# Optimization experiments

Measured on AMD Instinct MI355X. Metric: run time of the kernel, lower is better.

## Reference

```python
import jax, jax.numpy as jnp
import numpy as np

EPS = 1e-10            # safe_log epsilon
SIGMOID_BETA = 1.0
MLE_STEP_SIZE = 0.01
NUM_MLE_STEPS = 15
ENT_MULT = 0.01        # entropy loss multiplier placeholder
DECAY_MULT = 0.001     # weight decay multiplier placeholder
B, P, N, T = 512, 1024, 1024, 32


def sigmoid(a, beta=SIGMOID_BETA):
    # module's rescaled sigmoid: 2/(1+exp(-beta*a)) - 1, range (-1, 1)
    return 2.0 / (1.0 + jnp.exp(-beta * a)) - 1.0


def tri_basis(a_sig, centers):
    # triangle basis functions: relu(1 - |a - c_j| / width), width = center spacing
    # a_sig [B,N], centers [T] -> [B,N,T]
    width = centers[1] - centers[0]
    return jax.nn.relu(1.0 - jnp.abs(a_sig[..., None] - centers) / width)


def prob_est(a_sig, thetas, centers):
    # per-neuron mixture of triangle kernels; mixture weights = softmax(thetas)
    pi = jax.nn.softmax(thetas, axis=1)               # [N,T]
    return jnp.einsum('bnt,nt->bn', tri_basis(a_sig, centers), pi)  # [B,N]


def log_likelihood(a_sig, thetas, centers):
    return jnp.sum(jnp.log(prob_est(a_sig, thetas, centers) + EPS))


def calc_entropy(probs):
    # per-neuron entropy reduction over the batch axis
    return -jnp.sum(probs * jnp.log(probs + EPS), axis=0)  # [N]


def setup_inputs() -> dict:
    key = jax.random.key(0)
    k0, k1, k2, k3 = jax.random.split(key, 4)
    x = jax.random.normal(k0, (B, P), jnp.float32)
    w_enc = 0.5 * jax.random.normal(k1, (P, N), jnp.float32)   # truncated_normal std 0.5 approx
    b_enc = 0.1 * jax.random.normal(k2, (N,), jnp.float32)
    w_dec = jnp.transpose(w_enc)                                # initialized as w_enc^T
    b_dec = 0.1 * jax.random.normal(k3, (P,), jnp.float32)
    thetas = jnp.ones((N, T), jnp.float32)                      # construct_thetas init
    triangle_centers = jnp.linspace(-1.0, 1.0, T).astype(jnp.float32)  # a_sig range
    return {"x": x, "w_enc": w_enc, "b_enc": b_enc, "w_dec": w_dec,
            "b_dec": b_dec, "thetas": thetas, "triangle_centers": triangle_centers}


def reference(x, w_enc, b_enc, w_dec, b_dec, thetas, triangle_centers):
    # --- inference: relu encoder (noise_var_mult = 0 -> deterministic a) ---
    a = jax.nn.relu(x @ w_enc + b_enc)                # [B,N]
    a_sig = sigmoid(a, SIGMOID_BETA)                  # [B,N] in (-1,1)

    # --- iterative MLE gradient-ascent on thetas (num_mle_steps updates) ---
    ll_grad = jax.grad(lambda th: log_likelihood(a_sig, th, triangle_centers))

    def mle_step(th, _):
        return th + MLE_STEP_SIZE * ll_grad(th), None

    thetas_new, _ = jax.lax.scan(mle_step, thetas, None, length=NUM_MLE_STEPS)

    # --- entropy of the triangle-kernel density estimate ---
    probs = prob_est(a_sig, thetas_new, triangle_centers)   # [B,N]
    a_entropies = calc_entropy(probs)                       # [N]

    # --- decoder / losses ---
    x_hat = a @ w_dec + b_dec                               # [B,P]
    recon_loss = jnp.mean(0.5 * jnp.sum((x - x_hat) ** 2, axis=1))
    entropy_loss = ENT_MULT * jnp.sum(a_entropies)
    # tf.nn.l2_loss(t) = sum(t^2)/2
    decay_loss = 0.5 * DECAY_MULT * (0.5 * jnp.sum(w_enc ** 2) + 0.5 * jnp.sum(w_dec ** 2))
    total_loss = recon_loss + entropy_loss + decay_loss
    return x_hat, a_entropies, total_loss
```

## Files before the change

### kernel.cpp

```cpp
#include <hip/hip_runtime.h>

#define EPSC 1e-10f
#define BDIM 512
#define PDIM 1024
#define NDIM 1024
#define TDIM 32

typedef __attribute__((ext_vector_type(8))) short short8;
typedef __attribute__((ext_vector_type(4))) float f32x4;

static __device__ __forceinline__ short f2bf(float f) {
  unsigned u = __float_as_uint(f);
  unsigned r = (u + 0x7fffu + ((u >> 16) & 1u)) >> 16;
  return (short)r;
}

__global__ __launch_bounds__(256) void conv_x_kernel(
    const float* __restrict__ X, short* __restrict__ Xbf, float* __restrict__ accums)
{
  int tid = threadIdx.x;
  if (blockIdx.x == 0 && tid < 4) accums[tid] = 0.0f;
  size_t base = (size_t)blockIdx.x * 2048 + (size_t)tid * 8;
  float4 v0 = *(const float4*)(X + base);
  float4 v1 = *(const float4*)(X + base + 4);
  short8 o;
  o[0] = f2bf(v0.x); o[1] = f2bf(v0.y); o[2] = f2bf(v0.z); o[3] = f2bf(v0.w);
  o[4] = f2bf(v1.x); o[5] = f2bf(v1.y); o[6] = f2bf(v1.z); o[7] = f2bf(v1.w);
  *(short8*)(Xbf + base) = o;
}

__global__ __launch_bounds__(256) void conv_w_kernel(
    const float* __restrict__ W1, const float* __restrict__ W2,
    short* __restrict__ T1, short* __restrict__ T2, float* __restrict__ accums)
{
  __shared__ float T[64][65];
  __shared__ float red[4];
  const float* src = blockIdx.z ? W2 : W1;
  short* dst = blockIdx.z ? T2 : T1;
  int tid = threadIdx.x;
  int r0 = blockIdx.y * 64;
  int c0 = blockIdx.x * 64;
  float wsq = 0.0f;
#pragma unroll
  for (int i = 0; i < 4; ++i) {
    int row = (tid >> 4) + i * 16;
    int col = (tid & 15) << 2;
    float4 v = *(const float4*)(src + (size_t)(r0 + row) * NDIM + c0 + col);
    T[row][col + 0] = v.x; T[row][col + 1] = v.y; T[row][col + 2] = v.z; T[row][col + 3] = v.w;
    wsq = fmaf(v.x, v.x, wsq); wsq = fmaf(v.y, v.y, wsq);
    wsq = fmaf(v.z, v.z, wsq); wsq = fmaf(v.w, v.w, wsq);
  }
  __syncthreads();
  int n = tid >> 2;
  int kb = (tid & 3) << 4;
  short8 o0, o1;
#pragma unroll
  for (int i = 0; i < 8; ++i) o0[i] = f2bf(T[kb + i][n]);
#pragma unroll
  for (int i = 0; i < 8; ++i) o1[i] = f2bf(T[kb + 8 + i][n]);
  short* dp = dst + (size_t)(c0 + n) * NDIM + r0 + kb;
  *(short8*)dp = o0;
  *(short8*)(dp + 8) = o1;
#pragma unroll
  for (int d = 32; d >= 1; d >>= 1) wsq += __shfl_xor(wsq, d);
  if ((tid & 63) == 0) red[tid >> 6] = wsq;
  __syncthreads();
  if (tid == 0) atomicAdd(accums + 2, red[0] + red[1] + red[2] + red[3]);
}

__global__ __launch_bounds__(256) void gemm1_mfma(
    const short* __restrict__ Xbf, const short* __restrict__ WT,
    const float* __restrict__ bias, const float* __restrict__ centers,
    short* __restrict__ Abf, float* __restrict__ U)
{
  int tid = threadIdx.x;
  int lane = tid & 63, wid = tid >> 6;
  int q = lane >> 4, r16 = lane & 15;
  int bn = blockIdx.x * 32;
  int m = blockIdx.y * 64 + wid * 16 + r16;
  const short* ap  = Xbf + (size_t)m * NDIM + q * 8;
  const short* b0p = WT + (size_t)(bn + r16) * NDIM + q * 8;
  const short* b1p = b0p + 16 * NDIM;
  f32x4 acc0 = {0.f, 0.f, 0.f, 0.f};
  f32x4 acc1 = {0.f, 0.f, 0.f, 0.f};
#pragma unroll 4
  for (int k = 0; k < NDIM; k += 32) {
    short8 a  = *(const short8*)(ap + k);
    short8 b0 = *(const short8*)(b0p + k);
    short8 b1 = *(const short8*)(b1p + k);
    acc0 = __builtin_amdgcn_mfma_f32_16x16x32_bf16(a, b0, acc0, 0, 0, 0);
    acc1 = __builtin_amdgcn_mfma_f32_16x16x32_bf16(a, b1, acc1, 0, 0, 0);
  }
  float c0 = centers[0];
  float invw = 1.0f / (centers[1] - centers[0]);
  int mrow = blockIdx.y * 64 + wid * 16 + (q << 2);
  int n0 = bn + r16;
  float bi0 = bias[n0], bi1 = bias[n0 + 16];
#pragma unroll
  for (int r = 0; r < 4; ++r) {
    int mm = mrow + r;
    float a0 = fmaxf(acc0[r] + bi0, 0.0f);
    float a1 = fmaxf(acc1[r] + bi1, 0.0f);
    Abf[(size_t)mm * NDIM + n0]      = f2bf(a0);
    Abf[(size_t)mm * NDIM + n0 + 16] = f2bf(a1);
    U[(size_t)n0 * BDIM + mm]        = (2.0f / (1.0f + __expf(-a0)) - 1.0f - c0) * invw;
    U[(size_t)(n0 + 16) * BDIM + mm] = (2.0f / (1.0f + __expf(-a1)) - 1.0f - c0) * invw;
  }
}

__global__ __launch_bounds__(256) void gemm2_mfma(
    const short* __restrict__ Abf, const short* __restrict__ WdT,
    const float* __restrict__ bias, const float* __restrict__ X,
    float* __restrict__ out, float* __restrict__ accums)
{
  __shared__ float red[4];
  int tid = threadIdx.x;
  int lane = tid & 63, wid = tid >> 6;
  int q = lane >> 4, r16 = lane & 15;
  int bn = blockIdx.x * 32;
  int m = blockIdx.y * 64 + wid * 16 + r16;
  const short* ap  = Abf + (size_t)m * NDIM + q * 8;
  const short* b0p = WdT + (size_t)(bn + r16) * NDIM + q * 8;
  const short* b1p = b0p + 16 * NDIM;
  f32x4 acc0 = {0.f, 0.f, 0.f, 0.f};
  f32x4 acc1 = {0.f, 0.f, 0.f, 0.f};
#pragma unroll 4
  for (int k = 0; k < NDIM; k += 32) {
    short8 a  = *(const short8*)(ap + k);
    short8 b0 = *(const short8*)(b0p + k);
    short8 b1 = *(const short8*)(b1p + k);
    acc0 = __builtin_amdgcn_mfma_f32_16x16x32_bf16(a, b0, acc0, 0, 0, 0);
    acc1 = __builtin_amdgcn_mfma_f32_16x16x32_bf16(a, b1, acc1, 0, 0, 0);
  }
  int mrow = blockIdx.y * 64 + wid * 16 + (q << 2);
  int p0 = bn + r16;
  float bi0 = bias[p0], bi1 = bias[p0 + 16];
  float local = 0.0f;
#pragma unroll
  for (int r = 0; r < 4; ++r) {
    int mm = mrow + r;
    float xh0 = acc0[r] + bi0;
    float xh1 = acc1[r] + bi1;
    out[(size_t)mm * PDIM + p0]      = xh0;
    out[(size_t)mm * PDIM + p0 + 16] = xh1;
    float d0 = xh0 - X[(size_t)mm * PDIM + p0];
    float d1 = xh1 - X[(size_t)mm * PDIM + p0 + 16];
    local = fmaf(d0, d0, local);
    local = fmaf(d1, d1, local);
  }
#pragma unroll
  for (int d = 32; d >= 1; d >>= 1) local += __shfl_xor(local, d);
  if ((tid & 63) == 0) red[tid >> 6] = local;
  __syncthreads();
  if (tid == 0) atomicAdd(accums + 0, red[0] + red[1] + red[2] + red[3]);
}

__global__ __launch_bounds__(64) void mle_kernel(
    const float* __restrict__ U, const float* __restrict__ thetas,
    float* __restrict__ ent_out, float* __restrict__ accums)
{
  int n = blockIdx.x;
  int lane = threadIdx.x;
  __shared__ float th_s[TDIM];
  __shared__ float pi_s[TDIM];
  __shared__ float s_s[64 * 33];

  float f_reg[8];
  int j_reg[8];
#pragma unroll
  for (int i = 0; i < 8; i++) {
    float u = U[(size_t)n * BDIM + lane + i * 64];
    int j = (int)u;
    if (j > TDIM - 2) j = TDIM - 2;
    f_reg[i] = u - (float)j;
    j_reg[i] = j;
  }
  if (lane < TDIM) th_s[lane] = thetas[(size_t)n * TDIM + lane];
  __syncthreads();

  int h = lane >> 5, t = lane & 31;
  for (int step = 0; step < 15; ++step) {
    float tv = th_s[lane & 31];
    float mx = tv;
#pragma unroll
    for (int d = 16; d >= 1; d >>= 1) mx = fmaxf(mx, __shfl_xor(mx, d));
    float e = __expf(tv - mx);
    float se = e;
#pragma unroll
    for (int d = 16; d >= 1; d >>= 1) se += __shfl_xor(se, d);
    float pv = e / se;
    if (lane < TDIM) pi_s[lane] = pv;
#pragma unroll
    for (int i = 0; i < 33; i++) s_s[lane * 33 + i] = 0.0f;
    __syncthreads();

    float S_local = 0.0f;
#pragma unroll
    for (int i = 0; i < 8; i++) {
      int j = j_reg[i];
      float f = f_reg[i];
      float p = (1.0f - f) * pi_s[j] + f * pi_s[j + 1];
      float r = 1.0f / (p + EPSC);
      S_local = fmaf(p, r, S_local);
      float* sp = &s_s[lane * 33 + j];
      sp[0] += (1.0f - f) * r;
      sp[1] += f * r;
    }
    __syncthreads();
    float S = S_local;
#pragma unroll
    for (int d = 32; d >= 1; d >>= 1) S += __shfl_xor(S, d);
    float colsum = 0.0f;
#pragma unroll 8
    for (int L = 0; L < 32; ++L) colsum += s_s[(h * 32 + L) * 33 + t];
    colsum += __shfl_xor(colsum, 32);
    if (lane < TDIM) th_s[lane] += 0.01f * pv * (colsum - S);
    __syncthreads();
  }

  float tv = th_s[lane & 31];
  float mx = tv;
#pragma unroll
  for (int d = 16; d >= 1; d >>= 1) mx = fmaxf(mx, __shfl_xor(mx, d));
  float e = __expf(tv - mx);
  float se = e;
#pragma unroll
  for (int d = 16; d >= 1; d >>= 1) se += __shfl_xor(se, d);
  if (lane < TDIM) pi_s[lane] = e / se;
  __syncthreads();
  float ent_local = 0.0f;
#pragma unroll
  for (int i = 0; i < 8; i++) {
    int j = j_reg[i];
    float f = f_reg[i];
    float p = (1.0f - f) * pi_s[j] + f * pi_s[j + 1];
    ent_local = fmaf(p, __logf(p + EPSC), ent_local);
  }
  float E = ent_local;
#pragma unroll
  for (int d = 32; d >= 1; d >>= 1) E += __shfl_xor(E, d);
  if (lane == 0) {
    float entn = -E;
    ent_out[n] = entn;
    atomicAdd(accums + 1, entn);
  }
}

__global__ void finalize_kernel(const float* __restrict__ accums, float* __restrict__ out) {
  if (threadIdx.x == 0) {
    float recon = accums[0] * (0.5f / (float)BDIM);
    float entl = 0.01f * accums[1];
    float decay = 0.00025f * accums[2];
    out[(size_t)BDIM * PDIM + NDIM] = recon + entl + decay;
  }
}

extern "C" void kernel_launch(void* const* d_in, const int* in_sizes, int n_in,
                              void* d_out, int out_size, void* d_ws, size_t ws_size,
                              hipStream_t stream) {
  (void)in_sizes; (void)n_in; (void)out_size; (void)ws_size;
  const float* x       = (const float*)d_in[0];
  const float* w_enc   = (const float*)d_in[1];
  const float* b_enc   = (const float*)d_in[2];
  const float* w_dec   = (const float*)d_in[3];
  const float* b_dec   = (const float*)d_in[4];
  const float* thetas  = (const float*)d_in[5];
  const float* centers = (const float*)d_in[6];
  float* out = (float*)d_out;

  char* ws = (char*)d_ws;
  short* Xbf    = (short*)(ws);
  short* WT     = (short*)(ws + (1 << 20));
  short* WdT    = (short*)(ws + (3 << 20));
  short* Abf    = (short*)(ws + (5 << 20));
  float* accums = (float*)(ws + (6 << 20));
  float* U      = out;
  float* ent_out = out + (size_t)BDIM * PDIM;

  hipLaunchKernelGGL(conv_x_kernel, dim3(256), dim3(256), 0, stream, x, Xbf, accums);
  hipLaunchKernelGGL(conv_w_kernel, dim3(16, 16, 2), dim3(256), 0, stream,
                     w_enc, w_dec, WT, WdT, accums);
  hipLaunchKernelGGL(gemm1_mfma, dim3(32, 8), dim3(256), 0, stream,
                     Xbf, WT, b_enc, centers, Abf, U);
  hipLaunchKernelGGL(mle_kernel, dim3(NDIM), dim3(64), 0, stream, U, thetas, ent_out, accums);
  hipLaunchKernelGGL(gemm2_mfma, dim3(32, 8), dim3(256), 0, stream,
                     Abf, WdT, b_dec, x, out, accums);
  hipLaunchKernelGGL(finalize_kernel, dim3(1), dim3(64), 0, stream, accums, out);
}
```

Baseline: 152.4 us.

## Swizzle operands into MFMA fragment layout, merge conversions, and finalize loss via ticket

Converts X and both weight matrices in a single launch into a pre-swizzled tile layout that matches MFMA fragment order, so each GEMM lane reads one contiguous short8 per k-chunk. The GEMMs are retiled to one 16x16 tile per wave, doubling the grid. U now goes to workspace and is written through a shared-memory transpose with float4 stores. The MLE kernel drops shared-memory pi/theta buffers in favour of shuffles and uses a wider padded scratch layout. Atomics and the separate finalize kernel are replaced by per-block partial sums plus a last-block ticket reduction, removing two launches. The cost is more complex indexing and a ticket counter that gemm1 resets on every call.

New measurement: 159.0 us. +4.3%, slower.

```diff
diff --git a/kernel.cpp b/kernel.cpp
--- a/kernel.cpp
+++ b/kernel.cpp
@@ -15,31 +15,33 @@
   return (short)r;
 }
 
-__global__ __launch_bounds__(256) void conv_x_kernel(
-    const float* __restrict__ X, short* __restrict__ Xbf, float* __restrict__ accums)
+__global__ __launch_bounds__(256) void conv_kernel(
+    const float* __restrict__ X, const float* __restrict__ W1, const float* __restrict__ W2,
+    short* __restrict__ Xsw, short* __restrict__ T1, short* __restrict__ T2,
+    float* __restrict__ pwsq)
 {
   int tid = threadIdx.x;
-  if (blockIdx.x == 0 && tid < 4) accums[tid] = 0.0f;
-  size_t base = (size_t)blockIdx.x * 2048 + (size_t)tid * 8;
-  float4 v0 = *(const float4*)(X + base);
-  float4 v1 = *(const float4*)(X + base + 4);
-  short8 o;
-  o[0] = f2bf(v0.x); o[1] = f2bf(v0.y); o[2] = f2bf(v0.z); o[3] = f2bf(v0.w);
-  o[4] = f2bf(v1.x); o[5] = f2bf(v1.y); o[6] = f2bf(v1.z); o[7] = f2bf(v1.w);
-  *(short8*)(Xbf + base) = o;
-}
-
-__global__ __launch_bounds__(256) void conv_w_kernel(
-    const float* __restrict__ W1, const float* __restrict__ W2,
-    short* __restrict__ T1, short* __restrict__ T2, float* __restrict__ accums)
-{
+  if (blockIdx.x < 256) {
+    int i = blockIdx.x * 256 + tid;
+    int m = i >> 7, c = i & 127;
+    const float* src = X + (size_t)m * 1024 + c * 8;
+    float4 v0 = *(const float4*)src;
+    float4 v1 = *(const float4*)(src + 4);
+    short8 o;
+    o[0] = f2bf(v0.x); o[1] = f2bf(v0.y); o[2] = f2bf(v0.z); o[3] = f2bf(v0.w);
+    o[4] = f2bf(v1.x); o[5] = f2bf(v1.y); o[6] = f2bf(v1.z); o[7] = f2bf(v1.w);
+    *(short8*)(Xsw + ((size_t)((m >> 4) * 32 + (c >> 2)) * 512) + (c & 3) * 128 + (m & 15) * 8) = o;
+    return;
+  }
   __shared__ float T[64][65];
   __shared__ float red[4];
-  const float* src = blockIdx.z ? W2 : W1;
-  short* dst = blockIdx.z ? T2 : T1;
-  int tid = threadIdx.x;
-  int r0 = blockIdx.y * 64;
-  int c0 = blockIdx.x * 64;
+  int wb = blockIdx.x - 256;
+  int z = wb >> 8;
+  int w = wb & 255;
+  int r0 = (w >> 4) * 64;
+  int c0 = (w & 15) * 64;
+  const float* src = z ? W2 : W1;
+  short* dst = z ? T2 : T1;
   float wsq = 0.0f;
 #pragma unroll
   for (int i = 0; i < 4; ++i) {
@@ -51,119 +53,115 @@
     wsq = fmaf(v.z, v.z, wsq); wsq = fmaf(v.w, v.w, wsq);
   }
   __syncthreads();
-  int n = tid >> 2;
+  int nl = tid >> 2;
   int kb = (tid & 3) << 4;
-  short8 o0, o1;
-#pragma unroll
-  for (int i = 0; i < 8; ++i) o0[i] = f2bf(T[kb + i][n]);
-#pragma unroll
-  for (int i = 0; i < 8; ++i) o1[i] = f2bf(T[kb + 8 + i][n]);
-  short* dp = dst + (size_t)(c0 + n) * NDIM + r0 + kb;
-  *(short8*)dp = o0;
-  *(short8*)(dp + 8) = o1;
+  int ng = c0 + nl;
+  int nt = ng >> 4, rn = ng & 15;
+#pragma unroll
+  for (int h = 0; h < 2; ++h) {
+    int kg = r0 + kb + 8 * h;
+    int kc = kg >> 5, q = (kg >> 3) & 3;
+    short8 o;
+#pragma unroll
+    for (int e = 0; e < 8; ++e) o[e] = f2bf(T[kb + 8 * h + e][nl]);
+    *(short8*)(dst + ((size_t)(nt * 32 + kc) * 512) + q * 128 + rn * 8) = o;
+  }
 #pragma unroll
   for (int d = 32; d >= 1; d >>= 1) wsq += __shfl_xor(wsq, d);
   if ((tid & 63) == 0) red[tid >> 6] = wsq;
   __syncthreads();
-  if (tid == 0) atomicAdd(accums + 2, red[0] + red[1] + red[2] + red[3]);
+  if (tid == 0) pwsq[wb] = red[0] + red[1] + red[2] + red[3];
 }
 
 __global__ __launch_bounds__(256) void gemm1_mfma(
-    const short* __restrict__ Xbf, const short* __restrict__ WT,
+    const short* __restrict__ Xsw, const short* __restrict__ Wsw,
     const float* __restrict__ bias, const float* __restrict__ centers,
-    short* __restrict__ Abf, float* __restrict__ U)
-{
+    short* __restrict__ Absw, float* __restrict__ U, int* __restrict__ ticket)
+{
+  __shared__ float T2s[32][36];
   int tid = threadIdx.x;
+  if (blockIdx.x == 0 && blockIdx.y == 0 && tid == 0) *ticket = 0;
   int lane = tid & 63, wid = tid >> 6;
-  int q = lane >> 4, r16 = lane & 15;
-  int bn = blockIdx.x * 32;
-  int m = blockIdx.y * 64 + wid * 16 + r16;
-  const short* ap  = Xbf + (size_t)m * NDIM + q * 8;
-  const short* b0p = WT + (size_t)(bn + r16) * NDIM + q * 8;
-  const short* b1p = b0p + 16 * NDIM;
-  f32x4 acc0 = {0.f, 0.f, 0.f, 0.f};
-  f32x4 acc1 = {0.f, 0.f, 0.f, 0.f};
-#pragma unroll 4
-  for (int k = 0; k < NDIM; k += 32) {
-    short8 a  = *(const short8*)(ap + k);
-    short8 b0 = *(const short8*)(b0p + k);
-    short8 b1 = *(const short8*)(b1p + k);
-    acc0 = __builtin_amdgcn_mfma_f32_16x16x32_bf16(a, b0, acc0, 0, 0, 0);
-    acc1 = __builtin_amdgcn_mfma_f32_16x16x32_bf16(a, b1, acc1, 0, 0, 0);
-  }
+  int wy = wid >> 1, wx = wid & 1;
+  int mt = blockIdx.y * 2 + wy;
+  int nt = blockIdx.x * 2 + wx;
+  const short* ap = Xsw + (size_t)mt * 16384 + lane * 8;
+  const short* bp = Wsw + (size_t)nt * 16384 + lane * 8;
+  f32x4 acc = {0.f, 0.f, 0.f, 0.f};
+#pragma unroll 8
+  for (int kc = 0; kc < 32; ++kc) {
+    short8 a = *(const short8*)(ap + kc * 512);
+    short8 b = *(const short8*)(bp + kc * 512);
+    acc = __builtin_amdgcn_mfma_f32_16x16x32_bf16(a, b, acc, 0, 0, 0);
+  }
+  int q = lane >> 4, r = lane & 15;
+  int nn = nt * 16 + r;
+  float bi = bias[nn];
   float c0 = centers[0];
   float invw = 1.0f / (centers[1] - centers[0]);
-  int mrow = blockIdx.y * 64 + wid * 16 + (q << 2);
-  int n0 = bn + r16;
-  float bi0 = bias[n0], bi1 = bias[n0 + 16];
-#pragma unroll
-  for (int r = 0; r < 4; ++r) {
-    int mm = mrow + r;
-    float a0 = fmaxf(acc0[r] + bi0, 0.0f);
-    float a1 = fmaxf(acc1[r] + bi1, 0.0f);
-    Abf[(size_t)mm * NDIM + n0]      = f2bf(a0);
-    Abf[(size_t)mm * NDIM + n0 + 16] = f2bf(a1);
-    U[(size_t)n0 * BDIM + mm]        = (2.0f / (1.0f + __expf(-a0)) - 1.0f - c0) * invw;
-    U[(size_t)(n0 + 16) * BDIM + mm] = (2.0f / (1.0f + __expf(-a1)) - 1.0f - c0) * invw;
-  }
+  short* abase = Absw + ((size_t)(mt * 32 + (nn >> 5)) * 512) + ((nn >> 3) & 3) * 128 + (nn & 7);
+#pragma unroll
+  for (int rr = 0; rr < 4; ++rr) {
+    int rm = q * 4 + rr;
+    float a = fmaxf(acc[rr] + bi, 0.0f);
+    abase[rm * 8] = f2bf(a);
+    T2s[wx * 16 + r][wy * 16 + rm] = (2.0f / (1.0f + __expf(-a)) - 1.0f - c0) * invw;
+  }
+  __syncthreads();
+  int row = tid >> 3;
+  int col4 = (tid & 7) << 2;
+  float4 uv = make_float4(T2s[row][col4], T2s[row][col4 + 1], T2s[row][col4 + 2], T2s[row][col4 + 3]);
+  *(float4*)(U + (size_t)(blockIdx.x * 32 + row) * BDIM + blockIdx.y * 32 + col4) = uv;
 }
 
 __global__ __launch_bounds__(256) void gemm2_mfma(
-    const short* __restrict__ Abf, const short* __restrict__ WdT,
+    const short* __restrict__ Absw, const short* __restrict__ Wdsw,
     const float* __restrict__ bias, const float* __restrict__ X,
-    float* __restrict__ out, float* __restrict__ accums)
+    float* __restrict__ out, float* __restrict__ precon)
 {
   __shared__ float red[4];
   int tid = threadIdx.x;
   int lane = tid & 63, wid = tid >> 6;
-  int q = lane >> 4, r16 = lane & 15;
-  int bn = blockIdx.x * 32;
-  int m = blockIdx.y * 64 + wid * 16 + r16;
-  const short* ap  = Abf + (size_t)m * NDIM + q * 8;
-  const short* b0p = WdT + (size_t)(bn + r16) * NDIM + q * 8;
-  const short* b1p = b0p + 16 * NDIM;
-  f32x4 acc0 = {0.f, 0.f, 0.f, 0.f};
-  f32x4 acc1 = {0.f, 0.f, 0.f, 0.f};
-#pragma unroll 4
-  for (int k = 0; k < NDIM; k += 32) {
-    short8 a  = *(const short8*)(ap + k);
-    short8 b0 = *(const short8*)(b0p + k);
-    short8 b1 = *(const short8*)(b1p + k);
-    acc0 = __builtin_amdgcn_mfma_f32_16x16x32_bf16(a, b0, acc0, 0, 0, 0);
-    acc1 = __builtin_amdgcn_mfma_f32_16x16x32_bf16(a, b1, acc1, 0, 0, 0);
-  }
-  int mrow = blockIdx.y * 64 + wid * 16 + (q << 2);
-  int p0 = bn + r16;
-  float bi0 = bias[p0], bi1 = bias[p0 + 16];
+  int wy = wid >> 1, wx = wid & 1;
+  int mt = blockIdx.y * 2 + wy;
+  int nt = blockIdx.x * 2 + wx;
+  const short* ap = Absw + (size_t)mt * 16384 + lane * 8;
+  const short* bp = Wdsw + (size_t)nt * 16384 + lane * 8;
+  f32x4 acc = {0.f, 0.f, 0.f, 0.f};
+#pragma unroll 8
+  for (int kc = 0; kc < 32; ++kc) {
+    short8 a = *(const short8*)(ap + kc * 512);
+    short8 b = *(const short8*)(bp + kc * 512);
+    acc = __builtin_amdgcn_mfma_f32_16x16x32_bf16(a, b, acc, 0, 0, 0);
+  }
+  int q = lane >> 4, r = lane & 15;
+  int nn = nt * 16 + r;
+  float bi = bias[nn];
   float local = 0.0f;
 #pragma unroll
-  for (int r = 0; r < 4; ++r) {
-    int mm = mrow + r;
-    float xh0 = acc0[r] + bi0;
-    float xh1 = acc1[r] + bi1;
-    out[(size_t)mm * PDIM + p0]      = xh0;
-    out[(size_t)mm * PDIM + p0 + 16] = xh1;
-    float d0 = xh0 - X[(size_t)mm * PDIM + p0];
-    float d1 = xh1 - X[(size_t)mm * PDIM + p0 + 16];
-    local = fmaf(d0, d0, local);
-    local = fmaf(d1, d1, local);
+  for (int rr = 0; rr < 4; ++rr) {
+    int mm = mt * 16 + q * 4 + rr;
+    float xh = acc[rr] + bi;
+    out[(size_t)mm * PDIM + nn] = xh;
+    float d = xh - X[(size_t)mm * PDIM + nn];
+    local = fmaf(d, d, local);
   }
 #pragma unroll
   for (int d = 32; d >= 1; d >>= 1) local += __shfl_xor(local, d);
   if ((tid & 63) == 0) red[tid >> 6] = local;
   __syncthreads();
-  if (tid == 0) atomicAdd(accums + 0, red[0] + red[1] + red[2] + red[3]);
+  if (tid == 0) precon[blockIdx.y * 32 + blockIdx.x] = red[0] + red[1] + red[2] + red[3];
 }
 
 __global__ __launch_bounds__(64) void mle_kernel(
     const float* __restrict__ U, const float* __restrict__ thetas,
-    float* __restrict__ ent_out, float* __restrict__ accums)
+    float* __restrict__ ent_out, const float* __restrict__ precon,
+    const float* __restrict__ pwsq, int* __restrict__ ticket, float* __restrict__ out)
 {
   int n = blockIdx.x;
   int lane = threadIdx.x;
-  __shared__ float th_s[TDIM];
-  __shared__ float pi_s[TDIM];
-  __shared__ float s_s[64 * 33];
+  __shared__ float s_s[128 * 34];
+  __shared__ int tick_s;
 
   float f_reg[8];
   int j_reg[8];
@@ -172,15 +170,19 @@
     float u = U[(size_t)n * BDIM + lane + i * 64];
     int j = (int)u;
     if (j > TDIM - 2) j = TDIM - 2;
+    if (j < 0) j = 0;
     f_reg[i] = u - (float)j;
     j_reg[i] = j;
   }
-  if (lane < TDIM) th_s[lane] = thetas[(size_t)n * TDIM + lane];
-  __syncthreads();
-
+  float th = (lane < TDIM) ? thetas[(size_t)n * TDIM + lane] : 0.0f;
+
+  int base0 = lane * 34;
+  int base1 = (lane + 64) * 34;
   int h = lane >> 5, t = lane & 31;
+  float pv = 0.0f;
+
   for (int step = 0; step < 15; ++step) {
-    float tv = th_s[lane & 31];
+    float tv = __shfl(th, lane & 31);
     float mx = tv;
 #pragma unroll
     for (int d = 16; d >= 1; d >>= 1) mx = fmaxf(mx, __shfl_xor(mx, d));
@@ -188,21 +190,23 @@
     float se = e;
 #pragma unroll
     for (int d = 16; d >= 1; d >>= 1) se += __shfl_xor(se, d);
-    float pv = e / se;
-    if (lane < TDIM) pi_s[lane] = pv;
-#pragma unroll
-    for (int i = 0; i < 33; i++) s_s[lane * 33 + i] = 0.0f;
-    __syncthreads();
-
+    pv = e / se;
+#pragma unroll
+    for (int i = 0; i < 17; i++) {
+      *(float2*)&s_s[base0 + 2 * i] = make_float2(0.f, 0.f);
+      *(float2*)&s_s[base1 + 2 * i] = make_float2(0.f, 0.f);
+    }
     float S_local = 0.0f;
 #pragma unroll
     for (int i = 0; i < 8; i++) {
       int j = j_reg[i];
       float f = f_reg[i];
-      float p = (1.0f - f) * pi_s[j] + f * pi_s[j + 1];
+      float pj  = __shfl(pv, j);
+      float pj1 = __shfl(pv, j + 1);
+      float p = (1.0f - f) * pj + f * pj1;
       float r = 1.0f / (p + EPSC);
       S_local = fmaf(p, r, S_local);
-      float* sp = &s_s[lane * 33 + j];
+      float* sp = &s_s[(i < 4 ? base0 : base1) + j];
       sp[0] += (1.0f - f) * r;
       sp[1] += f * r;
     }
@@ -212,13 +216,13 @@
     for (int d = 32; d >= 1; d >>= 1) S += __shfl_xor(S, d);
     float colsum = 0.0f;
 #pragma unroll 8
-    for (int L = 0; L < 32; ++L) colsum += s_s[(h * 32 + L) * 33 + t];
+    for (int L = 0; L < 64; ++L) colsum += s_s[(h * 64 + L) * 34 + t];
     colsum += __shfl_xor(colsum, 32);
-    if (lane < TDIM) th_s[lane] += 0.01f * pv * (colsum - S);
+    if (lane < TDIM) th += 0.01f * pv * (colsum - S);
     __syncthreads();
   }
 
-  float tv = th_s[lane & 31];
+  float tv = __shfl(th, lane & 31);
   float mx = tv;
 #pragma unroll
   for (int d = 16; d >= 1; d >>= 1) mx = fmaxf(mx, __shfl_xor(mx, d));
@@ -226,32 +230,36 @@
   float se = e;
 #pragma unroll
   for (int d = 16; d >= 1; d >>= 1) se += __shfl_xor(se, d);
-  if (lane < TDIM) pi_s[lane] = e / se;
-  __syncthreads();
+  pv = e / se;
   float ent_local = 0.0f;
 #pragma unroll
   for (int i = 0; i < 8; i++) {
     int j = j_reg[i];
     float f = f_reg[i];
-    float p = (1.0f - f) * pi_s[j] + f * pi_s[j + 1];
+    float p = (1.0f - f) * __shfl(pv, j) + f * __shfl(pv, j + 1);
     ent_local = fmaf(p, __logf(p + EPSC), ent_local);
   }
   float E = ent_local;
 #pragma unroll
   for (int d = 32; d >= 1; d >>= 1) E += __shfl_xor(E, d);
-  if (lane == 0) {
-    float entn = -E;
-    ent_out[n] = entn;
-    atomicAdd(accums + 1, entn);
-  }
-}
-
-__global__ void finalize_kernel(const float* __restrict__ accums, float* __restrict__ out) {
-  if (threadIdx.x == 0) {
-    float recon = accums[0] * (0.5f / (float)BDIM);
-    float entl = 0.01f * accums[1];
-    float decay = 0.00025f * accums[2];
-    out[(size_t)BDIM * PDIM + NDIM] = recon + entl + decay;
+  if (lane == 0) ent_out[n] = -E;
+
+  __threadfence();
+  if (lane == 0) tick_s = atomicAdd(ticket, 1);
+  __syncthreads();
+  if (tick_s == NDIM - 1) {
+    __threadfence();
+    const volatile float* ev = (const volatile float*)ent_out;
+    float acc = 0.0f;
+#pragma unroll
+    for (int i = 0; i < 16; i++) acc += 0.01f * ev[lane + i * 64];
+#pragma unroll
+    for (int i = 0; i < 8; i++) acc += (0.5f / (float)BDIM) * precon[lane + i * 64];
+#pragma unroll
+    for (int i = 0; i < 8; i++) acc += 0.00025f * pwsq[lane + i * 64];
+#pragma unroll
+    for (int d = 32; d >= 1; d >>= 1) acc += __shfl_xor(acc, d);
+    if (lane == 0) out[(size_t)BDIM * PDIM + NDIM] = acc;
   }
 }
 
@@ -269,21 +277,22 @@
   float* out = (float*)d_out;
 
   char* ws = (char*)d_ws;
-  short* Xbf    = (short*)(ws);
-  short* WT     = (short*)(ws + (1 << 20));
-  short* WdT    = (short*)(ws + (3 << 20));
-  short* Abf    = (short*)(ws + (5 << 20));
-  float* accums = (float*)(ws + (6 << 20));
-  float* U      = out;
+  short* Xsw    = (short*)(ws);
+  short* Wsw    = (short*)(ws + (1 << 20));
+  short* Wdsw   = (short*)(ws + (3 << 20));
+  short* Absw   = (short*)(ws + (5 << 20));
+  float* U      = (float*)(ws + (6 << 20));
+  float* precon = (float*)(ws + (8 << 20));
+  float* pwsq   = (float*)(ws + (8 << 20) + 4096);
+  int*   ticket = (int*)(ws + (8 << 20) + 8192);
   float* ent_out = out + (size_t)BDIM * PDIM;
 
-  hipLaunchKernelGGL(conv_x_kernel, dim3(256), dim3(256), 0, stream, x, Xbf, accums);
-  hipLaunchKernelGGL(conv_w_kernel, dim3(16, 16, 2), dim3(256), 0, stream,
-                     w_enc, w_dec, WT, WdT, accums);
-  hipLaunchKernelGGL(gemm1_mfma, dim3(32, 8), dim3(256), 0, stream,
-                     Xbf, WT, b_enc, centers, Abf, U);
-  hipLaunchKernelGGL(mle_kernel, dim3(NDIM), dim3(64), 0, stream, U, thetas, ent_out, accums);
-  hipLaunchKernelGGL(gemm2_mfma, dim3(32, 8), dim3(256), 0, stream,
-                     Abf, WdT, b_dec, x, out, accums);
-  hipLaunchKernelGGL(finalize_kernel, dim3(1), dim3(64), 0, stream, accums, out);
-}
+  hipLaunchKernelGGL(conv_kernel, dim3(768), dim3(256), 0, stream,
+                     x, w_enc, w_dec, Xsw, Wsw, Wdsw, pwsq);
+  hipLaunchKernelGGL(gemm1_mfma, dim3(32, 16), dim3(256), 0, stream,
+                     Xsw, Wsw, b_enc, centers, Absw, U, ticket);
+  hipLaunchKernelGGL(gemm2_mfma, dim3(32, 16), dim3(256), 0, stream,
+                     Absw, Wdsw, b_dec, x, out, precon);
+  hipLaunchKernelGGL(mle_kernel, dim3(NDIM), dim3(64), 0, stream,
+                     U, thetas, ent_out, precon, pwsq, ticket, out);
+}
```
